# Kernel tuning notes

Measured on AMD Instinct MI355X. Metric: run time of the kernel, lower is better.

The kernel has to match this reference:

```python
import jax, jax.numpy as jnp
import numpy as np

PIXEL_THRESHOLD = 0.4
FRACTION_THRESHOLD = 0.03
NUM_CLASSES = 20  # cls_idx in [0, 20)
N, H, W = 100, 640, 1280


def setup_inputs() -> dict:
    key = jax.random.key(0)
    k1, k2, k3 = jax.random.split(key, 3)
    cls_prob = jax.random.uniform(k1, (N,), dtype=jnp.float32)
    mask_prob = jax.random.normal(k2, (N, H, W), dtype=jnp.float32)
    cls_idx = jax.random.randint(k3, (N,), 0, NUM_CLASSES, dtype=jnp.int32)
    return {"cls_prob": cls_prob, "mask_prob": mask_prob, "cls_idx": cls_idx}


def reference(cls_prob, mask_prob, cls_idx):
    """Greedy confidence-sorted panoptic mask merging (mask_removal).

    Returns:
      keep:       [N] bool  - whether each (sorted) instance was kept
      kept_masks: [N,H,W]   - assigned raw mask probs (zeros where suppressed/unassigned)
      order:      [N] int   - descending-confidence permutation applied
    """
    # Sort by class confidence, descending (matches np.argsort(...)[::-1])
    order = jnp.argsort(cls_prob)[::-1]
    mp_raw = mask_prob[order]                      # [N,H,W] pre-softmax copy
    mp_soft = jax.nn.softmax(mp_raw, axis=0)       # softmax across instances per pixel
    ci = cls_idx[order]                            # [N]

    h, w = mp_raw.shape[-2:]
    pan0 = jnp.zeros((h, w), dtype=mp_raw.dtype)            # panoptic_image
    mimg0 = jnp.zeros((NUM_CLASSES + 1, h, w), dtype=mp_raw.dtype)  # per-class mask_image

    def step(carry, inp):
        pan, mimg = carry
        prob_s, prob_raw, cidx = inp
        logit = (prob_s >= PIXEL_THRESHOLD).astype(prob_s.dtype)  # binarized mask
        mask_sum = logit.sum()
        curr = mimg[cidx]                                         # [H,W]
        overlap_cnt = ((curr >= 1) & (logit == 1)).sum().astype(prob_s.dtype)
        overlap = overlap_cnt / jnp.maximum(mask_sum, 1.0)
        trivial = logit.max() == logit.min()  # all-zero or all-one mask
        keep = (~trivial) & (mask_sum > 0) & (overlap <= FRACTION_THRESHOLD)
        assign = (pan == 0) & (logit == 1) & keep                 # unclaimed pixels
        kept_mask = jnp.where(assign, prob_raw, 0.0)
        pan = jnp.where(assign, 1.0, pan)
        mimg = mimg.at[cidx].add(jnp.where(assign, logit, 0.0))
        return (pan, mimg), (keep, kept_mask)

    (_, _), (keep, kept_masks) = jax.lax.scan(step, (pan0, mimg0), (mp_soft, mp_raw, ci))
    return keep, kept_masks, order
```

## Files before the change

kernel.cpp:

```cpp
#include <hip/hip_runtime.h>

#define N_INST 100
#define HW_PIX 819200
#define NPAIR (N_INST * N_INST)

struct alignas(16) Ent { int p; int ab; float ra; float rb; };

__global__ __launch_bounds__(128) void k0_sort(
    const float* __restrict__ cls_prob,
    const int* __restrict__ cls_idx,
    int* __restrict__ order,
    int* __restrict__ cls_sorted,
    float* __restrict__ out_order,
    unsigned int* __restrict__ nc,
    unsigned int* __restrict__ masksum,
    unsigned int* __restrict__ paircnt) {
  int t = threadIdx.x;
  if (t == 0) *nc = 0u;
  for (int i = t; i < N_INST; i += 128) masksum[i] = 0u;
  for (int i = t; i < NPAIR; i += 128) paircnt[i] = 0u;

  __shared__ float v[N_INST];
  __shared__ int ordl[N_INST];
  if (t < N_INST) v[t] = cls_prob[t];
  __syncthreads();
  if (t < N_INST) {
    float mv = v[t];
    int r = 0;
    for (int j = 0; j < N_INST; ++j) {
      float vj = v[j];
      r += (vj > mv) || (vj == mv && j > t);
    }
    ordl[r] = t;
  }
  __syncthreads();
  if (t < N_INST) {
    int o = ordl[t];
    order[t] = o;
    cls_sorted[t] = cls_idx[o];
    out_order[t] = (float)o;
  }
}

__device__ __forceinline__ void exact_pixel(
    int p, float m,
    const float* __restrict__ mp,
    const int* __restrict__ order,
    unsigned int* __restrict__ masksum,
    unsigned int* __restrict__ paircnt,
    unsigned int* __restrict__ nc,
    Ent* __restrict__ list) {
  float denom = 0.0f, e1 = -1.0f, e2 = -1.0f, r1 = 0.0f, r2 = 0.0f;
  int s1 = 0, s2 = 0;
  for (int k = 0; k < N_INST; ++k) {
    float xv = mp[(size_t)order[k] * HW_PIX + p];
    float e = expf(xv - m);
    denom += e;
    if (e > e1)      { e2 = e1; s2 = s1; r2 = r1; e1 = e; s1 = k; r1 = xv; }
    else if (e > e2) { e2 = e;  s2 = k;  r2 = xv; }
  }
  bool c1 = (e1 / denom) >= 0.4f;
  bool c2 = (e2 / denom) >= 0.4f;
  if (c1) {
    int a = s1, b = 255;
    float ra = r1, rb = 0.0f;
    atomicAdd(&masksum[s1], 1u);
    if (c2) {
      atomicAdd(&masksum[s2], 1u);
      if (s2 < s1) { a = s2; ra = r2; b = s1; rb = r1; }
      else         { b = s2; rb = r2; }
      atomicAdd(&paircnt[a * N_INST + b], 1u);
    }
    unsigned idx = atomicAdd(nc, 1u);
    Ent e; e.p = p; e.ab = a | (b << 8); e.ra = ra; e.rb = rb;
    list[idx] = e;
  }
}

__global__ __launch_bounds__(256) void k1_cand(
    const float* __restrict__ mp,
    const int* __restrict__ order,
    unsigned int* __restrict__ masksum,
    unsigned int* __restrict__ paircnt,
    unsigned int* __restrict__ nc,
    Ent* __restrict__ list,
    float* __restrict__ out_masks) {
  const int p0 = (blockIdx.x * 256 + threadIdx.x) * 4;
  float4 mx = make_float4(-INFINITY, -INFINITY, -INFINITY, -INFINITY);
  float4 dn = make_float4(0.0f, 0.0f, 0.0f, 0.0f);
  const float4 z = make_float4(0.0f, 0.0f, 0.0f, 0.0f);
#pragma unroll
  for (int k = 0; k < N_INST; ++k) {
    const float4 x = *reinterpret_cast<const float4*>(
        &mp[(size_t)order[k] * HW_PIX + p0]);
    *reinterpret_cast<float4*>(&out_masks[(size_t)k * HW_PIX + p0]) = z;
    float nm;
    nm = fmaxf(mx.x, x.x); dn.x = dn.x * __expf(mx.x - nm) + __expf(x.x - nm); mx.x = nm;
    nm = fmaxf(mx.y, x.y); dn.y = dn.y * __expf(mx.y - nm) + __expf(x.y - nm); mx.y = nm;
    nm = fmaxf(mx.z, x.z); dn.z = dn.z * __expf(mx.z - nm) + __expf(x.z - nm); mx.z = nm;
    nm = fmaxf(mx.w, x.w); dn.w = dn.w * __expf(mx.w - nm) + __expf(x.w - nm); mx.w = nm;
  }
  const float GUARD = 2.51f;
  bool any = (dn.x <= GUARD) | (dn.y <= GUARD) | (dn.z <= GUARD) | (dn.w <= GUARD);
  if (__builtin_expect(any, 0)) {
    if (dn.x <= GUARD) exact_pixel(p0 + 0, mx.x, mp, order, masksum, paircnt, nc, list);
    if (dn.y <= GUARD) exact_pixel(p0 + 1, mx.y, mp, order, masksum, paircnt, nc, list);
    if (dn.z <= GUARD) exact_pixel(p0 + 2, mx.z, mp, order, masksum, paircnt, nc, list);
    if (dn.w <= GUARD) exact_pixel(p0 + 3, mx.w, mp, order, masksum, paircnt, nc, list);
  }
}

__global__ __launch_bounds__(256) void k2_keep(
    const unsigned int* __restrict__ paircnt,
    const unsigned int* __restrict__ masksum,
    const int* __restrict__ cls_sorted,
    unsigned long long* __restrict__ keepmask,
    float* __restrict__ out_keep) {
  __shared__ unsigned int pl[NPAIR];
  __shared__ unsigned int ms[N_INST];
  __shared__ int cl[N_INST];
  for (int i = threadIdx.x; i < NPAIR; i += 256) pl[i] = paircnt[i];
  if (threadIdx.x < N_INST) {
    ms[threadIdx.x] = masksum[threadIdx.x];
    cl[threadIdx.x] = cls_sorted[threadIdx.x];
  }
  __syncthreads();
  if (threadIdx.x < 64) {
    int l = threadIdx.x;
    int j2 = l + 64;
    int cA = cl[l];
    int cB = (j2 < N_INST) ? cl[j2] : -1;
    bool kA = false, kB = false;
    unsigned long long km0 = 0, km1 = 0;
    for (int s = 0; s < N_INST; ++s) {
      int cs = cl[s];
      unsigned int ov = 0;
      if (l < s && kA && cA == cs) ov += pl[l * N_INST + s];
      if (j2 < s && kB && cB == cs) ov += pl[j2 * N_INST + s];
#pragma unroll
      for (int off = 32; off >= 1; off >>= 1) ov += __shfl_xor((int)ov, off);
      unsigned int m_s = ms[s];
      float overlap = (float)ov / fmaxf((float)m_s, 1.0f);
      bool keep = (m_s > 0u) && (m_s < (unsigned)HW_PIX) && (overlap <= 0.03f);
      if (keep) { if (s < 64) km0 |= 1ull << s; else km1 |= 1ull << (s - 64); }
      if (s == l)  kA = keep;
      if (s == j2) kB = keep;
    }
    if (l == 0) { keepmask[0] = km0; keepmask[1] = km1; }
    out_keep[l] = kA ? 1.0f : 0.0f;
    if (j2 < N_INST) out_keep[j2] = kB ? 1.0f : 0.0f;
  }
}

__global__ __launch_bounds__(256) void k3_scatter(
    const unsigned int* __restrict__ nc,
    const Ent* __restrict__ list,
    const unsigned long long* __restrict__ keepmask,
    float* __restrict__ out_masks) {
  unsigned long long km0 = keepmask[0], km1 = keepmask[1];
  unsigned n = *nc;
  for (unsigned i = blockIdx.x * 256 + threadIdx.x; i < n; i += gridDim.x * 256) {
    Ent e = list[i];
    int a = e.ab & 0xFF;
    int b = (e.ab >> 8) & 0xFF;
    bool ka = (a < 64) ? (((km0 >> a) & 1ull) != 0)
                       : ((a < N_INST) && (((km1 >> (a - 64)) & 1ull) != 0));
    bool kb = (b < 64) ? (((km0 >> b) & 1ull) != 0)
                       : ((b < N_INST) && (((km1 >> (b - 64)) & 1ull) != 0));
    if (ka)      out_masks[(size_t)a * HW_PIX + e.p] = e.ra;
    else if (kb) out_masks[(size_t)b * HW_PIX + e.p] = e.rb;
  }
}

extern "C" void kernel_launch(void* const* d_in, const int* in_sizes, int n_in,
                              void* d_out, int out_size, void* d_ws, size_t ws_size,
                              hipStream_t stream) {
  const float* cls_prob = (const float*)d_in[0];
  const float* mp       = (const float*)d_in[1];
  const int*   cls_idx  = (const int*)d_in[2];
  float* out = (float*)d_out;

  char* ws = (char*)d_ws;
  int* order                   = (int*)(ws + 0);
  int* cls_sorted              = (int*)(ws + 400);
  unsigned long long* keepmask = (unsigned long long*)(ws + 800);
  unsigned int* nc             = (unsigned int*)(ws + 1024);
  unsigned int* masksum        = (unsigned int*)(ws + 2048);
  unsigned int* paircnt        = (unsigned int*)(ws + 4096);
  Ent* list                    = (Ent*)(ws + 65536);

  float* out_keep  = out;
  float* out_masks = out + N_INST;
  float* out_order = out + N_INST + (size_t)N_INST * HW_PIX;

  k0_sort<<<1, 128, 0, stream>>>(cls_prob, cls_idx, order, cls_sorted, out_order,
                                 nc, masksum, paircnt);
  k1_cand<<<HW_PIX / 1024, 256, 0, stream>>>(mp, order, masksum, paircnt, nc,
                                             list, out_masks);
  k2_keep<<<1, 256, 0, stream>>>(paircnt, masksum, cls_sorted, keepmask, out_keep);
  k3_scatter<<<128, 256, 0, stream>>>(nc, list, keepmask, out_masks);
}
```

Baseline: 686.8 us.

## Move output zeroing to memset and batch loads with non-online softmax sum

The zeroing of the output masks moves out of the candidate kernel into a hipMemsetAsync. The kernel now caches the order permutation in shared memory and processes 2 pixels per thread instead of 4, doubling the grid. Loads are issued in batches of 10 rows to raise memory-level parallelism, and the online max-rescaled softmax becomes a plain sum of exps scaled by exp(-max), with a guard that falls back to the exact path for large magnitudes. This cuts ALU work and may overlap memory traffic better, at the cost of an extra memset pass and some overflow risk handled by the fallback.

```diff
diff --git a/kernel.cpp b/kernel.cpp
--- a/kernel.cpp
+++ b/kernel.cpp
@@ -83,30 +83,34 @@
     unsigned int* __restrict__ masksum,
     unsigned int* __restrict__ paircnt,
     unsigned int* __restrict__ nc,
-    Ent* __restrict__ list,
-    float* __restrict__ out_masks) {
-  const int p0 = (blockIdx.x * 256 + threadIdx.x) * 4;
-  float4 mx = make_float4(-INFINITY, -INFINITY, -INFINITY, -INFINITY);
-  float4 dn = make_float4(0.0f, 0.0f, 0.0f, 0.0f);
-  const float4 z = make_float4(0.0f, 0.0f, 0.0f, 0.0f);
-#pragma unroll
-  for (int k = 0; k < N_INST; ++k) {
-    const float4 x = *reinterpret_cast<const float4*>(
-        &mp[(size_t)order[k] * HW_PIX + p0]);
-    *reinterpret_cast<float4*>(&out_masks[(size_t)k * HW_PIX + p0]) = z;
-    float nm;
-    nm = fmaxf(mx.x, x.x); dn.x = dn.x * __expf(mx.x - nm) + __expf(x.x - nm); mx.x = nm;
-    nm = fmaxf(mx.y, x.y); dn.y = dn.y * __expf(mx.y - nm) + __expf(x.y - nm); mx.y = nm;
-    nm = fmaxf(mx.z, x.z); dn.z = dn.z * __expf(mx.z - nm) + __expf(x.z - nm); mx.z = nm;
-    nm = fmaxf(mx.w, x.w); dn.w = dn.w * __expf(mx.w - nm) + __expf(x.w - nm); mx.w = nm;
-  }
+    Ent* __restrict__ list) {
+  __shared__ int ord_s[N_INST];
+  if (threadIdx.x < N_INST) ord_s[threadIdx.x] = order[threadIdx.x];
+  __syncthreads();
+  const int p0 = (blockIdx.x * 256 + threadIdx.x) * 2;
+  float mxa = -INFINITY, mxb = -INFINITY;
+  float sa = 0.0f, sb = 0.0f;
+#pragma unroll
+  for (int b = 0; b < 10; ++b) {
+    float2 x[10];
+#pragma unroll
+    for (int j = 0; j < 10; ++j)
+      x[j] = *reinterpret_cast<const float2*>(
+          &mp[(size_t)ord_s[b * 10 + j] * HW_PIX + p0]);
+#pragma unroll
+    for (int j = 0; j < 10; ++j) {
+      sa += __expf(x[j].x); mxa = fmaxf(mxa, x[j].x);
+      sb += __expf(x[j].y); mxb = fmaxf(mxb, x[j].y);
+    }
+  }
+  float da = sa * __expf(-mxa);
+  float db = sb * __expf(-mxb);
   const float GUARD = 2.51f;
-  bool any = (dn.x <= GUARD) | (dn.y <= GUARD) | (dn.z <= GUARD) | (dn.w <= GUARD);
-  if (__builtin_expect(any, 0)) {
-    if (dn.x <= GUARD) exact_pixel(p0 + 0, mx.x, mp, order, masksum, paircnt, nc, list);
-    if (dn.y <= GUARD) exact_pixel(p0 + 1, mx.y, mp, order, masksum, paircnt, nc, list);
-    if (dn.z <= GUARD) exact_pixel(p0 + 2, mx.z, mp, order, masksum, paircnt, nc, list);
-    if (dn.w <= GUARD) exact_pixel(p0 + 3, mx.w, mp, order, masksum, paircnt, nc, list);
+  bool ea = !(da > GUARD) || (fabsf(mxa) > 60.0f);
+  bool eb = !(db > GUARD) || (fabsf(mxb) > 60.0f);
+  if (__builtin_expect(ea || eb, 0)) {
+    if (ea) exact_pixel(p0 + 0, mxa, mp, order, masksum, paircnt, nc, list);
+    if (eb) exact_pixel(p0 + 1, mxb, mp, order, masksum, paircnt, nc, list);
   }
 }
 
@@ -193,10 +197,10 @@
   float* out_masks = out + N_INST;
   float* out_order = out + N_INST + (size_t)N_INST * HW_PIX;
 
+  hipMemsetAsync(out_masks, 0, (size_t)N_INST * HW_PIX * sizeof(float), stream);
   k0_sort<<<1, 128, 0, stream>>>(cls_prob, cls_idx, order, cls_sorted, out_order,
                                  nc, masksum, paircnt);
-  k1_cand<<<HW_PIX / 1024, 256, 0, stream>>>(mp, order, masksum, paircnt, nc,
-                                             list, out_masks);
+  k1_cand<<<HW_PIX / 512, 256, 0, stream>>>(mp, order, masksum, paircnt, nc, list);
   k2_keep<<<1, 256, 0, stream>>>(paircnt, masksum, cls_sorted, keepmask, out_keep);
   k3_scatter<<<128, 256, 0, stream>>>(nc, list, keepmask, out_masks);
 }
```

Result: faster. 653.9 us (-4.8%).
